# Optimization experiments

Measured on AMD Instinct MI355X. Metric: run time of the kernel, lower is better.

Reference implementation:

```python
import jax, jax.numpy as jnp
import numpy as np

# Static config matching init_kwargs
COUT, CIN, K = 64, 64, 3
PAD = K // 2  # padding=1


def setup_inputs() -> dict:
    key = jax.random.key(0)
    k1, k2, k3 = jax.random.split(key, 3)
    B, H, W, FH, FW, SC = 2, 256, 256, 16, 16, 128
    hyper_params = COUT * CIN * K * K  # 36864
    x = jax.random.normal(k1, (B, CIN, H, W), jnp.float32)
    s = jax.random.normal(k2, (B, SC, FH, FW), jnp.float32)
    s2w = jax.random.normal(k3, (hyper_params, SC), jnp.float32) * 0.02
    return {"x": x, "s": s, "s2w": s2w}


def reference(x, s, s2w):
    """HyperPatchConv2d forward: per-patch dynamically generated 3x3 conv.

    x:   [b, c, h, w]   input feature map
    s:   [b, sc, fh, fw] hypernetwork signal (one vector per patch)
    s2w: [P, sc]         signal2weights 1x1 conv (P = out*cin*k*k)
    """
    b, c, h, w = x.shape
    fh, fw = s.shape[-2:]
    ph, pw = h // fh, w // fw          # patch size
    kh, kw = ph + 2 * PAD, pw + 2 * PAD  # unfold window (patch + halo)

    # signal2weights: 1x1 conv -> per-patch flattened conv weight
    wflat = jnp.einsum('pc,bcfg->bfgp', s2w, s)            # [b,fh,fw,P]
    Wdyn = wflat.reshape(b, fh, fw, COUT, CIN, K, K)        # per-patch conv kernels

    # reflect-pad then unfold into overlapping (kh,kw) patches, stride (ph,pw)
    xp = jnp.pad(x, ((0, 0), (0, 0), (PAD, PAD), (PAD, PAD)), mode='reflect')
    idx_h = (jnp.arange(fh) * ph)[:, None] + jnp.arange(kh)[None, :]  # [fh,kh]
    idx_w = (jnp.arange(fw) * pw)[:, None] + jnp.arange(kw)[None, :]  # [fw,kw]
    patches = xp[:, :, idx_h][:, :, :, :, idx_w]            # [b,c,fh,kh,fw,kw]

    # extract KxK sliding windows inside each patch (valid conv, stride 1)
    wi = jnp.arange(ph)[:, None] + jnp.arange(K)[None, :]   # [ph,K]
    wj = jnp.arange(pw)[:, None] + jnp.arange(K)[None, :]   # [pw,K]
    win = patches[:, :, :, wi]                              # [b,c,fh,ph,K,fw,kw]
    win = win[:, :, :, :, :, :, wj]                         # [b,c,fh,ph,K,fw,pw,K]
    win = win.transpose(0, 2, 5, 1, 3, 4, 6, 7)             # [b,fh,fw,c,ph,K,pw,K]

    # per-patch dynamic conv
    out = jnp.einsum('bfgocij,bfgcpiqj->bfgopq', Wdyn, win)  # [b,fh,fw,o,ph,pw]

    # fold: non-overlapping reassembly (stride == patch size)
    return out.transpose(0, 3, 1, 4, 2, 5).reshape(b, COUT, h, w)
```

## Files before the change

### kernel.cpp

```cpp
#include <hip/hip_runtime.h>
#include <hip/hip_bf16.h>


#define C_OUT 64
#define C_IN  64
#define P_TOTAL 36864
#define N_PATCH 512
#define WSTR 72
#define GPLANE 1032
#define CSTR 136

typedef __bf16 bf16x8 __attribute__((ext_vector_type(8)));
typedef float  f32x4  __attribute__((ext_vector_type(4)));

__device__ __forceinline__ unsigned short f2bf(float f) {
  unsigned int u = __float_as_uint(f);
  u += 0x7fffu + ((u >> 16) & 1u);
  return (unsigned short)(u >> 16);
}

__global__ __launch_bounds__(256) void prep_s(
    const float* __restrict__ s, unsigned short* __restrict__ sT) {
  const int bb = blockIdx.x;
  const int fg = threadIdx.x;
  unsigned short* dst = sT + ((size_t)bb * 256 + fg) * 128;
  for (int k = 0; k < 128; k += 2) {
    const float a = s[(size_t)(bb * 128 + k) * 256 + fg];
    const float b = s[(size_t)(bb * 128 + k + 1) * 256 + fg];
    const unsigned int u = (unsigned int)f2bf(a) | ((unsigned int)f2bf(b) << 16);
    *(unsigned int*)(dst + k) = u;
  }
}

__global__ __launch_bounds__(256) void prep_x(
    const float* __restrict__ x, unsigned short* __restrict__ xT) {
  __shared__ unsigned short lds[256 * 68];
  const int bb = blockIdx.x >> 8;
  const int row = blockIdx.x & 255;
  const int t = threadIdx.x;
  const float* src = x + ((size_t)bb * 64) * 65536 + row * 256 + t;
  #pragma unroll 8
  for (int ci = 0; ci < 64; ++ci)
    lds[t * 68 + ci] = f2bf(src[(size_t)ci * 65536]);
  __syncthreads();
  unsigned short* dst = xT + ((size_t)(bb * 65536 + row * 256 + t)) * 64;
  #pragma unroll
  for (int k8 = 0; k8 < 8; ++k8) {
    const uint2 u0 = *(const uint2*)&lds[t * 68 + k8 * 8];
    const uint2 u1 = *(const uint2*)&lds[t * 68 + k8 * 8 + 4];
    *(uint4*)(dst + k8 * 8) = make_uint4(u0.x, u0.y, u1.x, u1.y);
  }
}

__global__ __launch_bounds__(256) void wgen_kernel(
    const float* __restrict__ s2w,
    const unsigned short* __restrict__ sT,
    unsigned short* __restrict__ wout)
{
  __shared__ unsigned short smem[2 * 16 * GPLANE];
  unsigned short* As = smem;
  unsigned short* Bs = smem + 16 * GPLANE;
  const int tid = threadIdx.x;
  const int m0 = blockIdx.x * 128;
  const int n0 = blockIdx.y * 128;

  const int fragidx = m0 >> 9;
  const int tap = fragidx >> 3;
  const int ksH = (fragidx >> 2) & 1;
  const int mtH = fragidx & 3;

  #pragma unroll
  for (int i = 0; i < 8; ++i) {
    const int chunk = i * 256 + tid;
    const int row = chunk >> 4;
    const int g = chunk & 15;
    const int m = m0 + row;
    const int j = m & 7;
    const int lane6 = (m >> 3) & 63;
    const int co = mtH * 16 + (lane6 & 15);
    const int ci = ksH * 32 + (lane6 >> 4) * 8 + j;
    const int p = co * 576 + ci * 9 + tap;
    const float* src = s2w + (size_t)p * 128 + g * 8;
    const float4 v0 = *(const float4*)src;
    const float4 v1 = *(const float4*)(src + 4);
    uint4 o;
    o.x = (unsigned int)f2bf(v0.x) | ((unsigned int)f2bf(v0.y) << 16);
    o.y = (unsigned int)f2bf(v0.z) | ((unsigned int)f2bf(v0.w) << 16);
    o.z = (unsigned int)f2bf(v1.x) | ((unsigned int)f2bf(v1.y) << 16);
    o.w = (unsigned int)f2bf(v1.z) | ((unsigned int)f2bf(v1.w) << 16);
    *(uint4*)&As[g * GPLANE + row * 8] = o;
  }
  #pragma unroll
  for (int i = 0; i < 8; ++i) {
    const int chunk = i * 256 + tid;
    const int row = chunk >> 4;
    const int g = chunk & 15;
    *(uint4*)&Bs[g * GPLANE + row * 8] = *(const uint4*)(sT + ((size_t)(n0 + row)) * 128 + g * 8);
  }
  __syncthreads();

  const int wave = tid >> 6;
  const int lane = tid & 63;
  const int col = lane & 15;
  const int quad = lane >> 4;

  f32x4 acc[2][8] = {};
  #pragma unroll
  for (int ks = 0; ks < 4; ++ks) {
    const int g = ks * 4 + quad;
    bf16x8 afr[2], bfr[8];
    #pragma unroll
    for (int mti = 0; mti < 2; ++mti)
      afr[mti] = *(const bf16x8*)&As[g * GPLANE + ((wave * 2 + mti) * 16 + col) * 8];
    #pragma unroll
    for (int nt = 0; nt < 8; ++nt)
      bfr[nt] = *(const bf16x8*)&Bs[g * GPLANE + (nt * 16 + col) * 8];
    #pragma unroll
    for (int mti = 0; mti < 2; ++mti)
      #pragma unroll
      for (int nt = 0; nt < 8; ++nt)
        acc[mti][nt] = __builtin_amdgcn_mfma_f32_16x16x32_bf16(afr[mti], bfr[nt], acc[mti][nt], 0, 0, 0);
  }

  __syncthreads();
  unsigned short* Ct = smem;
  #pragma unroll
  for (int mti = 0; mti < 2; ++mti) {
    const int mloc = (wave * 2 + mti) * 16 + quad * 4;
    #pragma unroll
    for (int nt = 0; nt < 8; ++nt) {
      const int pl = nt * 16 + col;
      ushort4 o;
      o.x = f2bf(acc[mti][nt][0]); o.y = f2bf(acc[mti][nt][1]);
      o.z = f2bf(acc[mti][nt][2]); o.w = f2bf(acc[mti][nt][3]);
      *(ushort4*)&Ct[pl * CSTR + mloc] = o;
    }
  }
  __syncthreads();
  #pragma unroll
  for (int i = 0; i < 8; ++i) {
    const int chunk = i * 256 + tid;
    const int pl = chunk >> 4;
    const int ii = chunk & 15;
    const uint4 v = *(const uint4*)&Ct[pl * CSTR + ii * 8];
    *(uint4*)(wout + (size_t)(n0 + pl) * P_TOTAL + m0 + ii * 8) = v;
  }
}

__global__ __launch_bounds__(512) void conv_kernel(
    const unsigned short* __restrict__ xT,
    const unsigned short* __restrict__ wfrag,
    float* __restrict__ out)
{
  __shared__ unsigned short win[324 * WSTR];
  const int tid = threadIdx.x;
  const int patch = blockIdx.x;
  const int bb = patch >> 8;
  const int fg = patch & 255;
  const int f = fg >> 4, g = fg & 15;
  const int row0 = f * 16, col0 = g * 16;

  for (int chunk = tid; chunk < 2592; chunk += 512) {
    const int cell = chunk >> 3;
    const int j = chunk & 7;
    const int r = cell / 18;
    const int c = cell - r * 18;
    int rr = row0 + r - 1; rr = rr < 0 ? -rr : (rr > 255 ? 510 - rr : rr);
    int cc = col0 + c - 1; cc = cc < 0 ? -cc : (cc > 255 ? 510 - cc : cc);
    *(uint4*)&win[cell * WSTR + j * 8] =
        *(const uint4*)(xT + ((size_t)((bb << 16) + (rr << 8) + cc)) * 64 + j * 8);
  }
  __syncthreads();

  const int wave = tid >> 6;
  const int lane = tid & 63;
  const int t = lane & 15;
  const int quad = lane >> 4;

  f32x4 acc[4][2] = {};
  const bf16x8* wb = (const bf16x8*)(wfrag + (size_t)patch * P_TOTAL);

  for (int tap = 0; tap < 9; ++tap) {
    const int ti = tap / 3;
    const int tj = tap - ti * 3;
    bf16x8 afr[2][4];
    #pragma unroll
    for (int ks = 0; ks < 2; ++ks)
      #pragma unroll
      for (int mt = 0; mt < 4; ++mt)
        afr[ks][mt] = wb[((tap * 2 + ks) * 4 + mt) * 64 + lane];

    #pragma unroll
    for (int nt = 0; nt < 2; ++nt) {
      const int r = wave * 2 + nt + ti;
      const int c = t + tj;
      const int base = (r * 18 + c) * WSTR + quad * 8;
      #pragma unroll
      for (int ks = 0; ks < 2; ++ks) {
        const bf16x8 bfr = *(const bf16x8*)&win[base + ks * 32];
        #pragma unroll
        for (int mt = 0; mt < 4; ++mt)
          acc[mt][nt] = __builtin_amdgcn_mfma_f32_16x16x32_bf16(afr[ks][mt], bfr, acc[mt][nt], 0, 0, 0);
      }
    }
  }

  #pragma unroll
  for (int mt = 0; mt < 4; ++mt) {
    #pragma unroll
    for (int nt = 0; nt < 2; ++nt) {
      const int p = row0 + wave * 2 + nt;
      #pragma unroll
      for (int reg = 0; reg < 4; ++reg) {
        const int co = mt * 16 + quad * 4 + reg;
        out[(((size_t)bb * C_OUT + co) << 16) + ((size_t)p << 8) + col0 + t] = acc[mt][nt][reg];
      }
    }
  }
}

extern "C" void kernel_launch(void* const* d_in, const int* in_sizes, int n_in,
                              void* d_out, int out_size, void* d_ws, size_t ws_size,
                              hipStream_t stream) {
  const float* x   = (const float*)d_in[0];
  const float* s   = (const float*)d_in[1];
  const float* s2w = (const float*)d_in[2];
  float* out = (float*)d_out;

  char* ws = (char*)d_ws;
  unsigned short* wbuf = (unsigned short*)(ws);
  unsigned short* sT   = (unsigned short*)(ws + 37748736);
  unsigned short* xT   = (unsigned short*)(ws + 37879808);

  prep_s<<<2, 256, 0, stream>>>(s, sT);
  prep_x<<<512, 256, 0, stream>>>(x, xT);
  wgen_kernel<<<dim3(288, 4), 256, 0, stream>>>(s2w, sT, wbuf);
  conv_kernel<<<N_PATCH, 512, 0, stream>>>(xT, wbuf, out);
}
```

Measured before the change: 139.7 us.

## Merge prep kernels, reuse s2w tile across all N in wgen, remap conv waves

```diff
diff --git a/kernel.cpp b/kernel.cpp
--- a/kernel.cpp
+++ b/kernel.cpp
@@ -19,21 +19,9 @@
   return (unsigned short)(u >> 16);
 }
 
-__global__ __launch_bounds__(256) void prep_s(
-    const float* __restrict__ s, unsigned short* __restrict__ sT) {
-  const int bb = blockIdx.x;
-  const int fg = threadIdx.x;
-  unsigned short* dst = sT + ((size_t)bb * 256 + fg) * 128;
-  for (int k = 0; k < 128; k += 2) {
-    const float a = s[(size_t)(bb * 128 + k) * 256 + fg];
-    const float b = s[(size_t)(bb * 128 + k + 1) * 256 + fg];
-    const unsigned int u = (unsigned int)f2bf(a) | ((unsigned int)f2bf(b) << 16);
-    *(unsigned int*)(dst + k) = u;
-  }
-}
-
-__global__ __launch_bounds__(256) void prep_x(
-    const float* __restrict__ x, unsigned short* __restrict__ xT) {
+__global__ __launch_bounds__(256) void prep_xs(
+    const float* __restrict__ x, const float* __restrict__ s,
+    unsigned short* __restrict__ xT, unsigned short* __restrict__ sT) {
   __shared__ unsigned short lds[256 * 68];
   const int bb = blockIdx.x >> 8;
   const int row = blockIdx.x & 255;
@@ -50,6 +38,15 @@
     const uint2 u1 = *(const uint2*)&lds[t * 68 + k8 * 8 + 4];
     *(uint4*)(dst + k8 * 8) = make_uint4(u0.x, u0.y, u1.x, u1.y);
   }
+  if (blockIdx.x < 2) {
+    const int sb = blockIdx.x;
+    unsigned short* sd = sT + ((size_t)sb * 256 + t) * 128;
+    for (int k = 0; k < 128; k += 2) {
+      const float a = s[(size_t)(sb * 128 + k) * 256 + t];
+      const float b = s[(size_t)(sb * 128 + k + 1) * 256 + t];
+      *(unsigned int*)(sd + k) = (unsigned int)f2bf(a) | ((unsigned int)f2bf(b) << 16);
+    }
+  }
 }
 
 __global__ __launch_bounds__(256) void wgen_kernel(
@@ -57,12 +54,10 @@
     const unsigned short* __restrict__ sT,
     unsigned short* __restrict__ wout)
 {
-  __shared__ unsigned short smem[2 * 16 * GPLANE];
-  unsigned short* As = smem;
-  unsigned short* Bs = smem + 16 * GPLANE;
+  __shared__ unsigned short As[16 * GPLANE];
+  __shared__ unsigned short Bs[16 * GPLANE];
   const int tid = threadIdx.x;
   const int m0 = blockIdx.x * 128;
-  const int n0 = blockIdx.y * 128;
 
   const int fragidx = m0 >> 9;
   const int tap = fragidx >> 3;
@@ -80,9 +75,9 @@
     const int co = mtH * 16 + (lane6 & 15);
     const int ci = ksH * 32 + (lane6 >> 4) * 8 + j;
     const int p = co * 576 + ci * 9 + tap;
-    const float* src = s2w + (size_t)p * 128 + g * 8;
-    const float4 v0 = *(const float4*)src;
-    const float4 v1 = *(const float4*)(src + 4);
+    const float* srcp = s2w + (size_t)p * 128 + g * 8;
+    const float4 v0 = *(const float4*)srcp;
+    const float4 v1 = *(const float4*)(srcp + 4);
     uint4 o;
     o.x = (unsigned int)f2bf(v0.x) | ((unsigned int)f2bf(v0.y) << 16);
     o.y = (unsigned int)f2bf(v0.z) | ((unsigned int)f2bf(v0.w) << 16);
@@ -90,60 +85,68 @@
     o.w = (unsigned int)f2bf(v1.z) | ((unsigned int)f2bf(v1.w) << 16);
     *(uint4*)&As[g * GPLANE + row * 8] = o;
   }
-  #pragma unroll
-  for (int i = 0; i < 8; ++i) {
-    const int chunk = i * 256 + tid;
-    const int row = chunk >> 4;
-    const int g = chunk & 15;
-    *(uint4*)&Bs[g * GPLANE + row * 8] = *(const uint4*)(sT + ((size_t)(n0 + row)) * 128 + g * 8);
-  }
-  __syncthreads();
 
   const int wave = tid >> 6;
   const int lane = tid & 63;
   const int col = lane & 15;
   const int quad = lane >> 4;
 
-  f32x4 acc[2][8] = {};
-  #pragma unroll
-  for (int ks = 0; ks < 4; ++ks) {
-    const int g = ks * 4 + quad;
-    bf16x8 afr[2], bfr[8];
-    #pragma unroll
-    for (int mti = 0; mti < 2; ++mti)
-      afr[mti] = *(const bf16x8*)&As[g * GPLANE + ((wave * 2 + mti) * 16 + col) * 8];
-    #pragma unroll
-    for (int nt = 0; nt < 8; ++nt)
-      bfr[nt] = *(const bf16x8*)&Bs[g * GPLANE + (nt * 16 + col) * 8];
-    #pragma unroll
-    for (int mti = 0; mti < 2; ++mti)
+  for (int n0 = 0; n0 < 512; n0 += 128) {
+    #pragma unroll
+    for (int i = 0; i < 8; ++i) {
+      const int chunk = i * 256 + tid;
+      const int row = chunk >> 4;
+      const int g = chunk & 15;
+      *(uint4*)&Bs[g * GPLANE + row * 8] = *(const uint4*)(sT + ((size_t)(n0 + row)) * 128 + g * 8);
+    }
+    __syncthreads();
+
+    f32x4 acc[2][8] = {};
+    #pragma unroll
+    for (int ks = 0; ks < 4; ++ks) {
+      const int g = ks * 4 + quad;
+      bf16x8 afr[2], bfr[8];
+      #pragma unroll
+      for (int mti = 0; mti < 2; ++mti)
+        afr[mti] = *(const bf16x8*)&As[g * GPLANE + ((wave * 2 + mti) * 16 + col) * 8];
       #pragma unroll
       for (int nt = 0; nt < 8; ++nt)
-        acc[mti][nt] = __builtin_amdgcn_mfma_f32_16x16x32_bf16(afr[mti], bfr[nt], acc[mti][nt], 0, 0, 0);
-  }
-
-  __syncthreads();
-  unsigned short* Ct = smem;
-  #pragma unroll
-  for (int mti = 0; mti < 2; ++mti) {
-    const int mloc = (wave * 2 + mti) * 16 + quad * 4;
-    #pragma unroll
-    for (int nt = 0; nt < 8; ++nt) {
-      const int pl = nt * 16 + col;
-      ushort4 o;
-      o.x = f2bf(acc[mti][nt][0]); o.y = f2bf(acc[mti][nt][1]);
-      o.z = f2bf(acc[mti][nt][2]); o.w = f2bf(acc[mti][nt][3]);
-      *(ushort4*)&Ct[pl * CSTR + mloc] = o;
-    }
-  }
-  __syncthreads();
-  #pragma unroll
-  for (int i = 0; i < 8; ++i) {
-    const int chunk = i * 256 + tid;
-    const int pl = chunk >> 4;
-    const int ii = chunk & 15;
-    const uint4 v = *(const uint4*)&Ct[pl * CSTR + ii * 8];
-    *(uint4*)(wout + (size_t)(n0 + pl) * P_TOTAL + m0 + ii * 8) = v;
+        bfr[nt] = *(const bf16x8*)&Bs[g * GPLANE + (nt * 16 + col) * 8];
+      #pragma unroll
+      for (int mti = 0; mti < 2; ++mti)
+        #pragma unroll
+        for (int nt = 0; nt < 8; ++nt)
+          acc[mti][nt] = __builtin_amdgcn_mfma_f32_16x16x32_bf16(afr[mti], bfr[nt], acc[mti][nt], 0, 0, 0);
+    }
+    __syncthreads();
+
+    unsigned short* Ct = Bs;
+    #pragma unroll
+    for (int half = 0; half < 2; ++half) {
+      #pragma unroll
+      for (int mti = 0; mti < 2; ++mti) {
+        const int mloc = (wave * 2 + mti) * 16 + quad * 4;
+        #pragma unroll
+        for (int nt2 = 0; nt2 < 4; ++nt2) {
+          const int nt = half * 4 + nt2;
+          const int pl = nt2 * 16 + col;
+          ushort4 o;
+          o.x = f2bf(acc[mti][nt][0]); o.y = f2bf(acc[mti][nt][1]);
+          o.z = f2bf(acc[mti][nt][2]); o.w = f2bf(acc[mti][nt][3]);
+          *(ushort4*)&Ct[pl * CSTR + mloc] = o;
+        }
+      }
+      __syncthreads();
+      #pragma unroll
+      for (int i = 0; i < 4; ++i) {
+        const int chunk = i * 256 + tid;
+        const int pl = chunk >> 4;
+        const int ii = chunk & 15;
+        const uint4 v = *(const uint4*)&Ct[pl * CSTR + ii * 8];
+        *(uint4*)(wout + (size_t)(n0 + half * 64 + pl) * P_TOTAL + m0 + ii * 8) = v;
+      }
+      __syncthreads();
+    }
   }
 }
 
@@ -176,44 +179,46 @@
   const int lane = tid & 63;
   const int t = lane & 15;
   const int quad = lane >> 4;
-
-  f32x4 acc[4][2] = {};
+  const int mh = wave & 1;
+  const int rq = wave >> 1;
+
+  f32x4 acc[2][4] = {};
   const bf16x8* wb = (const bf16x8*)(wfrag + (size_t)patch * P_TOTAL);
 
+  #pragma unroll
   for (int tap = 0; tap < 9; ++tap) {
     const int ti = tap / 3;
     const int tj = tap - ti * 3;
-    bf16x8 afr[2][4];
+    bf16x8 afr[2][2];
     #pragma unroll
     for (int ks = 0; ks < 2; ++ks)
       #pragma unroll
-      for (int mt = 0; mt < 4; ++mt)
-        afr[ks][mt] = wb[((tap * 2 + ks) * 4 + mt) * 64 + lane];
-
-    #pragma unroll
-    for (int nt = 0; nt < 2; ++nt) {
-      const int r = wave * 2 + nt + ti;
+      for (int ml = 0; ml < 2; ++ml)
+        afr[ks][ml] = wb[((tap * 2 + ks) * 4 + mh * 2 + ml) * 64 + lane];
+
+    #pragma unroll
+    for (int nt = 0; nt < 4; ++nt) {
+      const int r = rq * 4 + nt + ti;
       const int c = t + tj;
       const int base = (r * 18 + c) * WSTR + quad * 8;
       #pragma unroll
       for (int ks = 0; ks < 2; ++ks) {
         const bf16x8 bfr = *(const bf16x8*)&win[base + ks * 32];
-        #pragma unroll
-        for (int mt = 0; mt < 4; ++mt)
-          acc[mt][nt] = __builtin_amdgcn_mfma_f32_16x16x32_bf16(afr[ks][mt], bfr, acc[mt][nt], 0, 0, 0);
-      }
-    }
-  }
-
-  #pragma unroll
-  for (int mt = 0; mt < 4; ++mt) {
-    #pragma unroll
-    for (int nt = 0; nt < 2; ++nt) {
-      const int p = row0 + wave * 2 + nt;
+        acc[0][nt] = __builtin_amdgcn_mfma_f32_16x16x32_bf16(afr[ks][0], bfr, acc[0][nt], 0, 0, 0);
+        acc[1][nt] = __builtin_amdgcn_mfma_f32_16x16x32_bf16(afr[ks][1], bfr, acc[1][nt], 0, 0, 0);
+      }
+    }
+  }
+
+  #pragma unroll
+  for (int ml = 0; ml < 2; ++ml) {
+    #pragma unroll
+    for (int nt = 0; nt < 4; ++nt) {
+      const int p = row0 + rq * 4 + nt;
       #pragma unroll
       for (int reg = 0; reg < 4; ++reg) {
-        const int co = mt * 16 + quad * 4 + reg;
-        out[(((size_t)bb * C_OUT + co) << 16) + ((size_t)p << 8) + col0 + t] = acc[mt][nt][reg];
+        const int co = (mh * 2 + ml) * 16 + quad * 4 + reg;
+        out[(((size_t)bb * C_OUT + co) << 16) + ((size_t)p << 8) + col0 + t] = acc[ml][nt][reg];
       }
     }
   }
@@ -232,8 +237,7 @@
   unsigned short* sT   = (unsigned short*)(ws + 37748736);
   unsigned short* xT   = (unsigned short*)(ws + 37879808);
 
-  prep_s<<<2, 256, 0, stream>>>(s, sT);
-  prep_x<<<512, 256, 0, stream>>>(x, xT);
-  wgen_kernel<<<dim3(288, 4), 256, 0, stream>>>(s2w, sT, wbuf);
+  prep_xs<<<512, 256, 0, stream>>>(x, s, xT, sT);
+  wgen_kernel<<<288, 256, 0, stream>>>(s2w, sT, wbuf);
   conv_kernel<<<N_PATCH, 512, 0, stream>>>(xT, wbuf, out);
 }
```

New measurement: 144.7 us. +3.6%, slower.
